# Kernel tuning notes

Measured on AMD Instinct MI355X. Metric: run time of the kernel, lower is better.

## Reference

```python
import jax, jax.numpy as jnp
import numpy as np

VIEWS = 16
TEMP = 0.07
BASE_TEMP = 0.07
EPS = 1e-12


def setup_inputs() -> dict:
    key = jax.random.key(0)
    k1, k2 = jax.random.split(key)
    features = jax.random.normal(k1, (8192, 128), dtype=jnp.float32)  # [bsz*views, d]
    labels = jax.random.randint(k2, (512,), 0, 100, dtype=jnp.int64 if jax.config.jax_enable_x64 else jnp.int32)
    return {"features": features, "labels": labels}


def reference(features, labels):
    bsz = labels.shape[0]                 # 512
    d = features.shape[-1]                # 128
    f = features.reshape(bsz, VIEWS, d)
    # F.normalize(p=2, dim=-1) with eps clamp
    norm = jnp.maximum(jnp.linalg.norm(f, axis=-1, keepdims=True), EPS)
    f = f / norm

    # positive mask from labels: [bsz, bsz]
    mask = (labels[:, None] == labels[None, :]).astype(jnp.float32)

    # contrast_feature = cat(unbind(f, dim=1)) -> view-major ordering
    contrast = jnp.transpose(f, (1, 0, 2)).reshape(VIEWS * bsz, d)  # [N, d]
    N = VIEWS * bsz

    # similarity logits, row-max stabilized (max is detached in torch)
    logits = jnp.matmul(contrast, contrast.T) / TEMP                 # [N, N]
    logits = logits - jax.lax.stop_gradient(jnp.max(logits, axis=1, keepdims=True))

    big_mask = jnp.tile(mask, (VIEWS, VIEWS))                        # [N, N]
    logits_mask = 1.0 - jnp.eye(N, dtype=jnp.float32)                # zero self-contrast
    big_mask = big_mask * logits_mask

    exp_logits = jnp.exp(logits) * logits_mask
    log_prob = logits - jnp.log(jnp.sum(exp_logits, axis=1, keepdims=True) + EPS)
    mean_log_prob_pos = jnp.sum(big_mask * log_prob, axis=1) / (jnp.sum(big_mask, axis=1) + EPS)

    loss = -(TEMP / BASE_TEMP) * mean_log_prob_pos                   # [N]
    return jnp.mean(loss.reshape(VIEWS, bsz))
```

## Files before the change

### kernel.cpp

```cpp
#include <hip/hip_runtime.h>
#include <hip/hip_bf16.h>

#define VIEWS 16
#define BSZ 512
#define NROWS 8192
#define D 128
#define CSPLIT 16
#define BCOLS 32
#define NSVC 100

typedef short bf16x8 __attribute__((ext_vector_type(8)));
typedef float f32x4 __attribute__((ext_vector_type(4)));

constexpr float C1 = 20.609929155556618f;
constexpr float INV_T = 14.285714285714286f;

__device__ __forceinline__ float bf2f(unsigned int u16) {
  return __uint_as_float(u16 << 16);
}

__device__ __forceinline__ unsigned short f2bf(float f) {
  unsigned int u = __float_as_uint(f);
  u += 0x7fffu + ((u >> 16) & 1u);
  return (unsigned short)(u >> 16);
}

__device__ __forceinline__ float fexp2(float x) {
#if __has_builtin(__builtin_amdgcn_exp2f)
  return __builtin_amdgcn_exp2f(x);
#else
  return exp2f(x);
#endif
}

__global__ __launch_bounds__(512) void k_norm_t(const float* __restrict__ feat,
                                                unsigned short* __restrict__ nrm,
                                                float* __restrict__ diag,
                                                float* __restrict__ T,
                                                float* __restrict__ out) {
  __shared__ float ldsT[VIEWS][D];
  int b = blockIdx.x;
  int t = threadIdx.x;
  if (b == 0 && t == 0) out[0] = 0.f;
  int v = t >> 5;
  int d0 = (t & 31) * 4;
  const float* src = feat + (size_t)(b * VIEWS + v) * D + d0;
  float4 x = *(const float4*)src;
  float ss = x.x * x.x + x.y * x.y + x.z * x.z + x.w * x.w;
#pragma unroll
  for (int m = 1; m < 32; m <<= 1) ss += __shfl_xor(ss, m);
  float inv = 1.0f / fmaxf(sqrtf(ss), 1e-12f);
  unsigned int u0 = f2bf(x.x * inv), u1 = f2bf(x.y * inv);
  unsigned int u2 = f2bf(x.z * inv), u3 = f2bf(x.w * inv);
  int n = v * BSZ + b;
  uint2 packed = {u0 | (u1 << 16), u2 | (u3 << 16)};
  *(uint2*)(nrm + (size_t)n * D + d0) = packed;
  float a0 = bf2f(u0), a1 = bf2f(u1), a2 = bf2f(u2), a3 = bf2f(u3);
  float ds = a0 * a0 + a1 * a1 + a2 * a2 + a3 * a3;
#pragma unroll
  for (int m = 1; m < 32; m <<= 1) ds += __shfl_xor(ds, m);
  if ((t & 31) == 0) diag[n] = ds;
  ldsT[v][d0] = a0;
  ldsT[v][d0 + 1] = a1;
  ldsT[v][d0 + 2] = a2;
  ldsT[v][d0 + 3] = a3;
  __syncthreads();
  if (t < D) {
    float acc = 0.f;
#pragma unroll
    for (int vv = 0; vv < VIEWS; ++vv) acc += ldsT[vv][t];
    T[(size_t)b * D + t] = acc;
  }
}

__global__ __launch_bounds__(512, 4) void k_gram_fused(
    const short* __restrict__ nrm, float* __restrict__ epart,
    const float* __restrict__ T, const int* __restrict__ labels,
    float* __restrict__ sv, int* __restrict__ cntc) {
  __shared__ __align__(16) char lds_raw[2][BCOLS][256];
  int tid = threadIdx.x;

  if (blockIdx.x < NSVC) {
    int* lab = (int*)&lds_raw[0][0][0];
    float* part = (float*)(&lds_raw[0][0][0] + 2048);
    int* pcnt = (int*)(&lds_raw[0][0][0] + 4096);
    int c = blockIdx.x;
    int q = tid >> 7;
    int d = tid & 127;
    lab[tid] = labels[tid];
    __syncthreads();
    float acc = 0.f;
    int count = 0;
#pragma unroll 4
    for (int b = q * 128; b < q * 128 + 128; ++b) {
      bool m = (lab[b] == c);
      float tv = T[(size_t)b * D + d];
      acc += m ? tv : 0.f;
      count += m ? 1 : 0;
    }
    part[q * D + d] = acc;
    if (d == 0) pcnt[q] = count;
    __syncthreads();
    if (tid < D) {
      sv[c * D + tid] = part[tid] + part[D + tid] + part[2 * D + tid] + part[3 * D + tid];
      if (tid == 0) cntc[c] = pcnt[0] + pcnt[1] + pcnt[2] + pcnt[3];
    }
    return;
  }

  int bid = blockIdx.x - NSVC;
  int rowblk = bid & 31;
  int cchunk = bid >> 5;
  int wid = tid >> 6;
  int lane = tid & 63;
  int idx = lane & 15;
  int kg = lane >> 4;
  int rowbase = rowblk * 256 + wid * 32;

  int srow = tid >> 4;
  int soff = (tid & 15) * 16;
  int swoff = srow * 256 + (soff ^ ((srow & 7) << 4));
  const char* gsrc = (const char*)nrm + (size_t)(cchunk * (NROWS / CSPLIT) + srow) * 256 + soff;

  bf16x8 afrag[2][4];
#pragma unroll
  for (int s = 0; s < 2; ++s)
#pragma unroll
    for (int c = 0; c < 4; ++c)
      afrag[s][c] = *(const bf16x8*)(nrm + (size_t)(rowbase + s * 16 + idx) * D + c * 32 + kg * 8);

  {
    uint4 v = *(const uint4*)gsrc;
    *(uint4*)(&lds_raw[0][0][0] + swoff) = v;
  }

  f32x4 eloc[2][2];
#pragma unroll
  for (int s = 0; s < 2; ++s)
#pragma unroll
    for (int g = 0; g < 2; ++g)
#pragma unroll
      for (int r = 0; r < 4; ++r) eloc[s][g][r] = 0.f;

  __syncthreads();

  const int NT = (NROWS / CSPLIT) / BCOLS;
  const int rdsw = (idx & 7) << 4;
#pragma unroll 1
  for (int t = 0; t < NT; ++t) {
    uint4 stage_v;
    if (t + 1 < NT) stage_v = *(const uint4*)(gsrc + (size_t)(t + 1) * BCOLS * 256);

    const char* buf = &lds_raw[t & 1][0][0];
    bf16x8 bfrag[2][4];
#pragma unroll
    for (int g = 0; g < 2; ++g)
#pragma unroll
      for (int c = 0; c < 4; ++c)
        bfrag[g][c] = *(const bf16x8*)(buf + (g * 16 + idx) * 256 + ((c * 64 + kg * 16) ^ rdsw));

#pragma unroll
    for (int s = 0; s < 2; ++s)
#pragma unroll
      for (int g = 0; g < 2; ++g) {
        f32x4 acc = {0.f, 0.f, 0.f, 0.f};
#pragma unroll
        for (int c = 0; c < 4; ++c)
          acc = __builtin_amdgcn_mfma_f32_16x16x32_bf16(afrag[s][c], bfrag[g][c], acc, 0, 0, 0);
#pragma unroll
        for (int r = 0; r < 4; ++r)
          eloc[s][g][r] += fexp2(acc[r] * C1 - C1);
      }

    if (t + 1 < NT) *(uint4*)(&lds_raw[(t + 1) & 1][0][0] + swoff) = stage_v;
    __syncthreads();
  }

#pragma unroll
  for (int s = 0; s < 2; ++s)
#pragma unroll
    for (int r = 0; r < 4; ++r) {
      float vv = eloc[s][0][r] + eloc[s][1][r];
      vv += __shfl_xor(vv, 1);
      vv += __shfl_xor(vv, 2);
      vv += __shfl_xor(vv, 4);
      vv += __shfl_xor(vv, 8);
      if (idx == 0)
        epart[(size_t)cchunk * NROWS + rowbase + s * 16 + kg * 4 + r] = vv;
    }
}

__global__ __launch_bounds__(256) void k_final(const unsigned int* __restrict__ nrm_u32,
                                               const float* __restrict__ diag,
                                               const float* __restrict__ epart,
                                               const float* __restrict__ sv,
                                               const int* __restrict__ labels,
                                               const int* __restrict__ cntc,
                                               float* __restrict__ out) {
  int w = threadIdx.x >> 6;
  int lane = threadIdx.x & 63;
  int wg = blockIdx.x * 4 + w;
  float lsum = 0.f;
#pragma unroll 1
  for (int i = 0; i < 16; ++i) {
    int n = wg * 16 + i;
    int b = n & (BSZ - 1);
    int lbl = labels[b];
    float2 s2 = *(const float2*)(sv + lbl * D + lane * 2);
    unsigned int u = nrm_u32[(size_t)n * (D / 2) + lane];
    float a0 = bf2f(u & 0xffffu), a1 = bf2f(u >> 16);
    float dot = a0 * s2.x + a1 * s2.y;
    float ep = (lane < CSPLIT) ? epart[(size_t)lane * NROWS + n] : 0.f;
#pragma unroll
    for (int m = 1; m < 64; m <<= 1) {
      dot += __shfl_xor(dot, m);
      ep += __shfl_xor(ep, m);
    }
    if (lane == 0) {
      float dii = diag[n];
      float Praw = dot - dii;
      float Cn = (float)(16 * cntc[lbl] - 1);
      float ediag = fexp2(dii * C1 - C1);
      float Eexcl = ep - ediag;
      float Sref = Eexcl * fexp2((1.0f - dii) * C1);
      float L = logf(Sref + 1e-12f);
      float mlpp = (Praw * INV_T - Cn * (dii * INV_T) - Cn * L) / (Cn + 1e-12f);
      lsum += -mlpp;
    }
  }
  __shared__ float part[4];
  if (lane == 0) part[w] = lsum;
  __syncthreads();
  if (threadIdx.x == 0)
    atomicAdd(out, (part[0] + part[1] + part[2] + part[3]) * (1.0f / NROWS));
}

extern "C" void kernel_launch(void* const* d_in, const int* in_sizes, int n_in,
                              void* d_out, int out_size, void* d_ws, size_t ws_size,
                              hipStream_t stream) {
  const float* feat = (const float*)d_in[0];
  const int* labels = (const int*)d_in[1];
  float* out = (float*)d_out;
  char* ws = (char*)d_ws;

  size_t off = 0;
  short* nrm = (short*)(ws + off);           off += (size_t)NROWS * D * 2;
  float* diag = (float*)(ws + off);          off += (size_t)NROWS * 4;
  float* epart = (float*)(ws + off);         off += (size_t)NROWS * CSPLIT * 4;
  float* sv = (float*)(ws + off);            off += (size_t)128 * D * 4;
  int* cntc = (int*)(ws + off);              off += (size_t)128 * 4;
  float* T = (float*)(ws + off);             off += (size_t)BSZ * D * 4;

  k_norm_t<<<BSZ, 512, 0, stream>>>(feat, (unsigned short*)nrm, diag, T, out);
  k_gram_fused<<<NSVC + 32 * CSPLIT, 512, 0, stream>>>(nrm, epart, T, labels, sv, cntc);
  k_final<<<128, 256, 0, stream>>>((const unsigned int*)nrm, diag, epart, sv, labels, cntc, out);
}
```

Before: 48.14 us.

## Exploit Gram matrix symmetry by computing only upper-triangular block pairs

Replaces the full row-block by column-chunk Gram sweep with a triangular enumeration of 256x256 block pairs (I<=J), which roughly halves the MFMA and exp work. Off-diagonal blocks also reduce column sums of exp through LDS and write them to a second partial buffer, and the final kernel gathers 32 partials per row from both buffers. This adds LDS traffic, extra shuffles, a serial loop to decode the pair index, and a larger partial workspace.

```diff
diff --git a/kernel.cpp b/kernel.cpp
--- a/kernel.cpp
+++ b/kernel.cpp
@@ -5,9 +5,10 @@
 #define BSZ 512
 #define NROWS 8192
 #define D 128
-#define CSPLIT 16
 #define BCOLS 32
 #define NSVC 100
+#define NBLK 32
+#define NPAIR 528
 
 typedef short bf16x8 __attribute__((ext_vector_type(8)));
 typedef float f32x4 __attribute__((ext_vector_type(4)));
@@ -74,10 +75,12 @@
 }
 
 __global__ __launch_bounds__(512, 4) void k_gram_fused(
-    const short* __restrict__ nrm, float* __restrict__ epart,
+    const short* __restrict__ nrm, float* __restrict__ epartA,
+    float* __restrict__ epartB,
     const float* __restrict__ T, const int* __restrict__ labels,
     float* __restrict__ sv, int* __restrict__ cntc) {
   __shared__ __align__(16) char lds_raw[2][BCOLS][256];
+  __shared__ float lds_col[8][256];
   int tid = threadIdx.x;
 
   if (blockIdx.x < NSVC) {
@@ -109,18 +112,24 @@
   }
 
   int bid = blockIdx.x - NSVC;
-  int rowblk = bid & 31;
-  int cchunk = bid >> 5;
+  int I = 0;
+  {
+    int rem = bid, span = NBLK;
+    while (rem >= span) { rem -= span; ++I; --span; }
+    bid = I + rem;
+  }
+  int J = bid;
+
   int wid = tid >> 6;
   int lane = tid & 63;
   int idx = lane & 15;
   int kg = lane >> 4;
-  int rowbase = rowblk * 256 + wid * 32;
+  int rowbase = I * 256 + wid * 32;
 
   int srow = tid >> 4;
   int soff = (tid & 15) * 16;
   int swoff = srow * 256 + (soff ^ ((srow & 7) << 4));
-  const char* gsrc = (const char*)nrm + (size_t)(cchunk * (NROWS / CSPLIT) + srow) * 256 + soff;
+  const char* gsrc = (const char*)nrm + (size_t)(J * 256 + srow) * 256 + soff;
 
   bf16x8 afrag[2][4];
 #pragma unroll
@@ -144,8 +153,9 @@
 
   __syncthreads();
 
-  const int NT = (NROWS / CSPLIT) / BCOLS;
+  const int NT = 256 / BCOLS;
   const int rdsw = (idx & 7) << 4;
+  const bool offdiag = (I < J);
 #pragma unroll 1
   for (int t = 0; t < NT; ++t) {
     uint4 stage_v;
@@ -159,6 +169,7 @@
       for (int c = 0; c < 4; ++c)
         bfrag[g][c] = *(const bf16x8*)(buf + (g * 16 + idx) * 256 + ((c * 64 + kg * 16) ^ rdsw));
 
+    float csum0 = 0.f, csum1 = 0.f;
 #pragma unroll
     for (int s = 0; s < 2; ++s)
 #pragma unroll
@@ -168,9 +179,23 @@
         for (int c = 0; c < 4; ++c)
           acc = __builtin_amdgcn_mfma_f32_16x16x32_bf16(afrag[s][c], bfrag[g][c], acc, 0, 0, 0);
 #pragma unroll
-        for (int r = 0; r < 4; ++r)
-          eloc[s][g][r] += fexp2(acc[r] * C1 - C1);
+        for (int r = 0; r < 4; ++r) {
+          float e = fexp2(acc[r] * C1 - C1);
+          eloc[s][g][r] += e;
+          if (g == 0) csum0 += e; else csum1 += e;
+        }
       }
+
+    if (offdiag) {
+      csum0 += __shfl_xor(csum0, 16);
+      csum0 += __shfl_xor(csum0, 32);
+      csum1 += __shfl_xor(csum1, 16);
+      csum1 += __shfl_xor(csum1, 32);
+      if (kg == 0) {
+        lds_col[wid][t * 32 + idx] = csum0;
+        lds_col[wid][t * 32 + 16 + idx] = csum1;
+      }
+    }
 
     if (t + 1 < NT) *(uint4*)(&lds_raw[(t + 1) & 1][0][0] + swoff) = stage_v;
     __syncthreads();
@@ -186,13 +211,24 @@
       vv += __shfl_xor(vv, 4);
       vv += __shfl_xor(vv, 8);
       if (idx == 0)
-        epart[(size_t)cchunk * NROWS + rowbase + s * 16 + kg * 4 + r] = vv;
-    }
+        epartA[(size_t)J * NROWS + rowbase + s * 16 + kg * 4 + r] = vv;
+    }
+
+  if (offdiag) {
+    __syncthreads();
+    if (tid < 256) {
+      float cv = 0.f;
+#pragma unroll
+      for (int w = 0; w < 8; ++w) cv += lds_col[w][tid];
+      epartB[(size_t)I * NROWS + J * 256 + tid] = cv;
+    }
+  }
 }
 
 __global__ __launch_bounds__(256) void k_final(const unsigned int* __restrict__ nrm_u32,
                                                const float* __restrict__ diag,
-                                               const float* __restrict__ epart,
+                                               const float* __restrict__ epartA,
+                                               const float* __restrict__ epartB,
                                                const float* __restrict__ sv,
                                                const int* __restrict__ labels,
                                                const int* __restrict__ cntc,
@@ -205,12 +241,18 @@
   for (int i = 0; i < 16; ++i) {
     int n = wg * 16 + i;
     int b = n & (BSZ - 1);
+    int K = n >> 8;
     int lbl = labels[b];
     float2 s2 = *(const float2*)(sv + lbl * D + lane * 2);
     unsigned int u = nrm_u32[(size_t)n * (D / 2) + lane];
     float a0 = bf2f(u & 0xffffu), a1 = bf2f(u >> 16);
     float dot = a0 * s2.x + a1 * s2.y;
-    float ep = (lane < CSPLIT) ? epart[(size_t)lane * NROWS + n] : 0.f;
+    float ep = 0.f;
+    if (lane < 32) {
+      int nA = 32 - K;
+      ep = (lane < nA) ? epartA[(size_t)(K + lane) * NROWS + n]
+                       : epartB[(size_t)(lane - nA) * NROWS + n];
+    }
 #pragma unroll
     for (int m = 1; m < 64; m <<= 1) {
       dot += __shfl_xor(dot, m);
@@ -246,12 +288,13 @@
   size_t off = 0;
   short* nrm = (short*)(ws + off);           off += (size_t)NROWS * D * 2;
   float* diag = (float*)(ws + off);          off += (size_t)NROWS * 4;
-  float* epart = (float*)(ws + off);         off += (size_t)NROWS * CSPLIT * 4;
+  float* epartA = (float*)(ws + off);        off += (size_t)NBLK * NROWS * 4;
+  float* epartB = (float*)(ws + off);        off += (size_t)NBLK * NROWS * 4;
   float* sv = (float*)(ws + off);            off += (size_t)128 * D * 4;
   int* cntc = (int*)(ws + off);              off += (size_t)128 * 4;
   float* T = (float*)(ws + off);             off += (size_t)BSZ * D * 4;
 
   k_norm_t<<<BSZ, 512, 0, stream>>>(feat, (unsigned short*)nrm, diag, T, out);
-  k_gram_fused<<<NSVC + 32 * CSPLIT, 512, 0, stream>>>(nrm, epart, T, labels, sv, cntc);
-  k_final<<<128, 256, 0, stream>>>((const unsigned int*)nrm, diag, epart, sv, labels, cntc, out);
-}
+  k_gram_fused<<<NSVC + NPAIR, 512, 0, stream>>>(nrm, epartA, epartB, T, labels, sv, cntc);
+  k_final<<<128, 256, 0, stream>>>((const unsigned int*)nrm, diag, epartA, epartB, sv, labels, cntc, out);
+}
```

After: 49.74 us. 1.03x slower.
